# Kernel tuning notes

Hardware: AMD Instinct MI355X
Metric: run time of the kernel (lower is better)

## Reference

```python
import jax, jax.numpy as jnp
import numpy as np

SCALE = 768.0  # scale = output_features


def setup_inputs() -> dict:
    key = jax.random.key(0)
    k1, k2, k3, k4 = jax.random.split(key, 4)
    B, S, D, F = 8, 2048, 768, 768
    x = jax.random.normal(k1, (B, S, D), dtype=jnp.float32)
    # torch nn.Linear weights: shape (out_features, in_features), y = x @ W.T
    Wq = jax.random.normal(k2, (F, D), dtype=jnp.float32) * (1.0 / np.sqrt(D))
    Wk = jax.random.normal(k3, (F, D), dtype=jnp.float32) * (1.0 / np.sqrt(D))
    Wv = jax.random.normal(k4, (F, D), dtype=jnp.float32) * (1.0 / np.sqrt(D))
    return {"x": x, "Wq": Wq, "Wk": Wk, "Wv": Wv}


def _cdist_l2(q, k):
    # pairwise Euclidean distances, [B, S, S]; matches torch.cdist(q, k, p=2)
    q2 = jnp.sum(q * q, axis=-1)  # [B, S]
    k2 = jnp.sum(k * k, axis=-1)  # [B, S]
    qk = jnp.einsum('bid,bjd->bij', q, k)  # [B, S, S]
    d2 = q2[:, :, None] + k2[:, None, :] - 2.0 * qk
    return jnp.sqrt(jnp.maximum(d2, 0.0))


def reference(x, Wq, Wk, Wv):
    q = jnp.einsum('bsd,fd->bsf', x, Wq)
    k = jnp.einsum('bsd,fd->bsf', x, Wk)
    v = jnp.einsum('bsd,fd->bsf', x, Wv)
    scores = _cdist_l2(q, k) / jnp.sqrt(jnp.asarray(SCALE, dtype=x.dtype))
    attn = jax.nn.softmax(scores, axis=-1)  # NOTE: source softmaxes raw distances (no negation)
    return jnp.einsum('bij,bjf->bif', attn, v)
```

## Files before the change

### kernel.cpp

```cpp
#include <hip/hip_runtime.h>
#include <hip/hip_fp8.h>
#include <stdint.h>
#include <math.h>


typedef __attribute__((ext_vector_type(8))) __bf16 bf16x8;
typedef __attribute__((ext_vector_type(4))) float f32x4;
typedef __attribute__((ext_vector_type(4))) unsigned int u32x4;
typedef __attribute__((ext_vector_type(2))) unsigned int u32x2;

__device__ __forceinline__ unsigned short f2b(float f) {
    unsigned u = __float_as_uint(f);
    unsigned r = 0x7fffu + ((u >> 16) & 1u);
    return (unsigned short)((u + r) >> 16);
}
__device__ __forceinline__ float b2f(unsigned short h) {
    return __uint_as_float(((unsigned)h) << 16);
}
__device__ __forceinline__ unsigned char f2f8(float f) {
    __hip_fp8_e4m3 t(f);
    return t.__x;
}
__device__ __forceinline__ float f8tof(unsigned char b) {
    int e = (b >> 3) & 15, m = b & 7;
    float v = e ? ldexpf(8.0f + m, e - 10) : ldexpf((float)m, -9);
    return (b & 0x80) ? -v : v;
}

__device__ __forceinline__ void wg_barrier() {
    asm volatile("" ::: "memory");
    __builtin_amdgcn_s_barrier();
    asm volatile("" ::: "memory");
}

__device__ __forceinline__ unsigned lds_off(const void* p) {
    return (unsigned)(uintptr_t)(const __attribute__((address_space(3))) char*)p;
}

__global__ __launch_bounds__(256) void castk(const float* __restrict__ src,
                                             unsigned short* __restrict__ dst, int n4) {
    int i = blockIdx.x * 256 + threadIdx.x;
    if (i >= n4) return;
    float4 v = ((const float4*)src)[i];
    ushort4 o;
    o.x = f2b(v.x); o.y = f2b(v.y); o.z = f2b(v.z); o.w = f2b(v.w);
    ((ushort4*)dst)[i] = o;
}

template <int MODE>
__global__ __launch_bounds__(256) void rowreduce(const unsigned short* __restrict__ X,
                                                 int L, int rows, float* __restrict__ out) {
    int w = threadIdx.x >> 6, lane = threadIdx.x & 63;
    int row = blockIdx.x * 4 + w;
    if (row >= rows) return;
    const unsigned short* xr = X + (size_t)row * L;
    float s = 0.f;
    int passes = L >> 8;
    for (int p = 0; p < passes; ++p) {
        ushort4 u = *(const ushort4*)(xr + (p << 8) + lane * 4);
        float a = b2f(u.x), b = b2f(u.y), c = b2f(u.z), d = b2f(u.w);
        s += MODE ? (a * a + b * b + c * c + d * d) : (a + b + c + d);
    }
#pragma unroll
    for (int o = 32; o > 0; o >>= 1) s += __shfl_down(s, o);
    if (lane == 0) out[row] = s;
}

__global__ __launch_bounds__(256) void rowreduce8(const unsigned char* __restrict__ X,
                                                  int L, int rows, float* __restrict__ out) {
    int w = threadIdx.x >> 6, lane = threadIdx.x & 63;
    int row = blockIdx.x * 4 + w;
    if (row >= rows) return;
    const unsigned char* xr = X + (size_t)row * L;
    float s = 0.f;
    int passes = L >> 8;
    for (int p = 0; p < passes; ++p) {
        uchar4 u = *(const uchar4*)(xr + (p << 8) + lane * 4);
        float a = f8tof(u.x), b = f8tof(u.y), c = f8tof(u.z), d = f8tof(u.w);
        s += a * a + b * b + c * c + d * d;
    }
#pragma unroll
    for (int o = 32; o > 0; o >>= 1) s += __shfl_down(s, o);
    if (lane == 0) out[row] = s;
}

#define MF(A_, B_, C_) (C_) = __builtin_amdgcn_mfma_f32_16x16x32_bf16((A_), (B_), (C_), 0, 0, 0)
#define MF8(A_, B_, C_) (C_) = __builtin_amdgcn_mfma_f32_16x16x32_fp8_fp8((A_), (B_), (C_), 0, 0, 0)
#define DSR(dst_, a_, imm_) \
    asm volatile("ds_read_b128 %0, %1 offset:" #imm_ : "=v"(dst_) : "v"(a_))
#define DSR64(dst_, a_, imm_) \
    asm volatile("ds_read_b64 %0, %1 offset:" #imm_ : "=v"(dst_) : "v"(a_))
#define GL4(d_, p_) asm volatile("global_load_dwordx4 %0, %1, off" : "=v"(d_) : "v"(p_))
#define GL2(d_, p_) asm volatile("global_load_dwordx2 %0, %1, off" : "=v"(d_) : "v"(p_))
#define DSW(a_, imm_, d_) \
    asm volatile("ds_write_b128 %0, %1 offset:" #imm_ :: "v"(a_), "v"(d_) : "memory")
#define DSW64(a_, imm_, d_) \
    asm volatile("ds_write_b64 %0, %1 offset:" #imm_ :: "v"(a_), "v"(d_) : "memory")
#define LGKM(n_) asm volatile("s_waitcnt lgkmcnt(" #n_ ")" ::: "memory")
#define VMC0 asm volatile("s_waitcnt vmcnt(0)" ::: "memory")
#define SB0 __builtin_amdgcn_sched_barrier(0)

#define LOADT(T_) do {                                                     \
    const size_t ko_ = (size_t)(T_) * 64;                                  \
    GL4(ra0, pa + ko_);             GL4(ra1, pa + lda64 + ko_);            \
    GL4(ra2, pa + 2 * lda64 + ko_); GL4(ra3, pa + 3 * lda64 + ko_);        \
    GL4(rb0, pb + ko_);             GL4(rb1, pb + ldb64 + ko_);            \
    GL4(rb2, pb + 2 * ldb64 + ko_); GL4(rb3, pb + 3 * ldb64 + ko_);        \
} while (0)
#define WRITET(WB_) do {                                                   \
    const unsigned wa_ = wA + (WB_), wb2_ = wB + (WB_);                    \
    DSW(wa_, 0, ra0);     DSW(wa_, 8192, ra1);                             \
    DSW(wa_, 16384, ra2); DSW(wa_, 24576, ra3);                            \
    DSW(wb2_, 0, rb0);     DSW(wb2_, 8192, rb1);                           \
    DSW(wb2_, 16384, rb2); DSW(wb2_, 24576, rb3);                          \
} while (0)

template <int EPI>
__global__ __launch_bounds__(512, 2) void gemm256(
    const unsigned short* __restrict__ A, int lda, long long sA,
    const unsigned short* __restrict__ B, int ldb, long long sB,
    void* __restrict__ Cv, int ldc, long long sC,
    int Kd, int perm,
    const float* __restrict__ aux1, int sAux1) {
    __shared__ __attribute__((aligned(128))) unsigned short As[2 * 256 * 64];
    __shared__ __attribute__((aligned(128))) unsigned short Bs[2 * 256 * 64];

    const int z = perm ? blockIdx.x : blockIdx.z;
    const int jb = perm ? blockIdx.y : blockIdx.x;
    const int ib = perm ? blockIdx.z : blockIdx.y;
    const unsigned short* __restrict__ Ab = A + (size_t)z * sA;
    const unsigned short* __restrict__ Bb = B + (size_t)z * sB;
    const int i0 = ib * 256, j0 = jb * 256;
    const int tid = threadIdx.x;
    const int w = tid >> 6, lane = tid & 63;
    const int wr = w >> 2, wc = w & 3;
    const int c16 = lane & 15, kq = lane >> 4;

    const int lr0 = tid >> 3;
    const int clog0 = (tid & 7) ^ (lr0 & 7);
    const unsigned short* pa = Ab + (size_t)(i0 + lr0) * lda + clog0 * 8;
    const unsigned short* pb = Bb + (size_t)(j0 + lr0) * ldb + clog0 * 8;
    const size_t lda64 = (size_t)64 * lda, ldb64 = (size_t)64 * ldb;

    const unsigned wA = lds_off(As) + (unsigned)tid * 16;
    const unsigned wB = lds_off(Bs) + (unsigned)tid * 16;

    const int swc = (kq ^ (c16 & 7)) << 4;
    const unsigned adrA0 = lds_off(As) + (unsigned)(wr * 128 + c16) * 128 + swc;
    const unsigned adrA0x = adrA0 ^ 64u;
    const unsigned adrB0 = lds_off(Bs) + (unsigned)(wc * 64 + c16) * 128 + swc;
    const unsigned adrB0x = adrB0 ^ 64u;

    f32x4 acc[8][4];
    const f32x4 zero = {0.f, 0.f, 0.f, 0.f};
#pragma unroll
    for (int i = 0; i < 8; ++i)
#pragma unroll
        for (int j = 0; j < 4; ++j) acc[i][j] = zero;

    u32x4 ra0, ra1, ra2, ra3, rb0, rb1, rb2, rb3;
    bf16x8 aL[4][2], aH[4][2], bF[4][2];

    const int nt = Kd >> 6;

    LOADT(0);
    VMC0;
    WRITET(0u);
    LOADT(1);
    LGKM(0);
    wg_barrier();

    for (int t = 0; t < nt; ++t) {
        const unsigned rb_ = (t & 1) ? 32768u : 0u;
        const unsigned wb_ = (t & 1) ? 0u : 32768u;
        const unsigned aA = adrA0 + rb_, aAx = adrA0x + rb_;
        const unsigned aB = adrB0 + rb_, aBx = adrB0x + rb_;
        DSR(aL[0][0], aA, 0);    DSR(aL[0][1], aAx, 0);
        DSR(aL[1][0], aA, 2048); DSR(aL[1][1], aAx, 2048);
        DSR(aL[2][0], aA, 4096); DSR(aL[2][1], aAx, 4096);
        DSR(aL[3][0], aA, 6144); DSR(aL[3][1], aAx, 6144);
        DSR(bF[0][0], aB, 0);    DSR(bF[0][1], aBx, 0);
        DSR(bF[1][0], aB, 2048); DSR(bF[1][1], aBx, 2048);
        DSR(bF[2][0], aB, 4096); DSR(bF[2][1], aBx, 4096);
        DSR(bF[3][0], aB, 6144); DSR(bF[3][1], aBx, 6144);
        if (t + 1 < nt) {
            VMC0;
            WRITET(wb_);
            if (t + 2 < nt) LOADT(t + 2);
            LGKM(8);
        } else {
            LGKM(0);
        }
        SB0;
        __builtin_amdgcn_s_setprio(1);
#pragma unroll
        for (int kk = 0; kk < 2; ++kk)
#pragma unroll
            for (int mi = 0; mi < 4; ++mi)
#pragma unroll
                for (int ni = 0; ni < 4; ++ni)
                    MF(aL[mi][kk], bF[ni][kk], acc[mi][ni]);
        __builtin_amdgcn_s_setprio(0);
        DSR(aH[0][0], aA, 8192);  DSR(aH[0][1], aAx, 8192);
        DSR(aH[1][0], aA, 10240); DSR(aH[1][1], aAx, 10240);
        DSR(aH[2][0], aA, 12288); DSR(aH[2][1], aAx, 12288);
        DSR(aH[3][0], aA, 14336); DSR(aH[3][1], aAx, 14336);
        LGKM(0); SB0;
        __builtin_amdgcn_s_setprio(1);
#pragma unroll
        for (int kk = 0; kk < 2; ++kk)
#pragma unroll
            for (int mi = 0; mi < 4; ++mi)
#pragma unroll
                for (int ni = 0; ni < 4; ++ni)
                    MF(aH[mi][kk], bF[ni][kk], acc[4 + mi][ni]);
        __builtin_amdgcn_s_setprio(0);
        wg_barrier();
    }
    const int prow = kq * 4;
    if constexpr (EPI == 0) {
        unsigned short* C = (unsigned short*)Cv + (size_t)z * sC;
        unsigned short* sc = (unsigned short*)((char*)As + w * 8192);
        const int rr = lane >> 3, ch = lane & 7;
#pragma unroll
        for (int mi = 0; mi < 8; ++mi) {
#pragma unroll
            for (int ni = 0; ni < 4; ++ni)
#pragma unroll
                for (int r = 0; r < 4; ++r)
                    sc[(prow + r) * 72 + ni * 16 + c16] = f2b(acc[mi][ni][r]);
#pragma unroll
            for (int pass = 0; pass < 2; ++pass) {
                const int r2 = rr + 8 * pass;
                bf16x8 v = *(const bf16x8*)&sc[r2 * 72 + ch * 8];
                const int grow = i0 + wr * 128 + mi * 16 + r2;
                *(bf16x8*)&C[(size_t)grow * ldc + j0 + wc * 64 + ch * 8] = v;
            }
        }
    } else if constexpr (EPI == 3) {
        unsigned char* C = (unsigned char*)Cv + (size_t)z * sC;
        unsigned char* sc = (unsigned char*)As + w * 8192;
        const int rr = lane >> 2, ch = lane & 3;
#pragma unroll
        for (int mi = 0; mi < 8; ++mi) {
#pragma unroll
            for (int ni = 0; ni < 4; ++ni)
#pragma unroll
                for (int r = 0; r < 4; ++r)
                    sc[(prow + r) * 80 + ni * 16 + c16] = f2f8(acc[mi][ni][r]);
            u32x4 v = *(const u32x4*)&sc[rr * 80 + ch * 16];
            const int grow = i0 + wr * 128 + mi * 16 + rr;
            *(u32x4*)&C[(size_t)grow * ldc + j0 + wc * 64 + ch * 16] = v;
        }
    } else {
        float* C = (float*)Cv + (size_t)z * sC;
        const float* lb = aux1 + (size_t)z * sAux1;
        float* sc = (float*)((char*)As + w * 8192);
        const int rr = lane >> 4, ch = lane & 15;
#pragma unroll
        for (int mi = 0; mi < 8; ++mi) {
#pragma unroll
            for (int ni = 0; ni < 4; ++ni)
#pragma unroll
                for (int r = 0; r < 4; ++r) {
                    const int grow = i0 + wr * 128 + mi * 16 + prow + r;
                    sc[(prow + r) * 68 + ni * 16 + c16] = acc[mi][ni][r] / lb[grow];
                }
#pragma unroll
            for (int pass = 0; pass < 4; ++pass) {
                const int r2 = rr + 4 * pass;
                f32x4 v = *(const f32x4*)&sc[r2 * 68 + ch * 4];
                const int grow = i0 + wr * 128 + mi * 16 + r2;
                *(f32x4*)&C[(size_t)grow * ldc + j0 + wc * 64 + ch * 4] = v;
            }
        }
    }
}

#define LOADT8(T_) do {                                                    \
    const size_t ko_ = (size_t)(T_) * 64;                                  \
    GL2(fa0, pa8 + ko_);              GL2(fa1, pa8 + lda64b + ko_);        \
    GL2(fa2, pa8 + 2 * lda64b + ko_); GL2(fa3, pa8 + 3 * lda64b + ko_);    \
    GL2(fb0, pb8 + ko_);              GL2(fb1, pb8 + ldb64b + ko_);        \
    GL2(fb2, pb8 + 2 * ldb64b + ko_); GL2(fb3, pb8 + 3 * ldb64b + ko_);    \
} while (0)
#define WRITET8(WB_) do {                                                  \
    const unsigned wa_ = wA8 + (WB_), wb2_ = wB8 + (WB_);                  \
    DSW64(wa_, 0, fa0);     DSW64(wa_, 4096, fa1);                         \
    DSW64(wa_, 8192, fa2);  DSW64(wa_, 12288, fa3);                        \
    DSW64(wb2_, 0, fb0);    DSW64(wb2_, 4096, fb1);                        \
    DSW64(wb2_, 8192, fb2); DSW64(wb2_, 12288, fb3);                       \
} while (0)

__global__ __launch_bounds__(512, 2) void gemm256f8(
    const unsigned char* __restrict__ A, int lda, long long sA,
    const unsigned char* __restrict__ B, int ldb, long long sB,
    unsigned short* __restrict__ Cq, int ldc, long long sC,
    int Kd,
    const float* __restrict__ q2a, int sQ2,
    const float* __restrict__ k2a, int sK2,
    float invs) {
    __shared__ __attribute__((aligned(128))) unsigned char As8[2 * 256 * 64];
    __shared__ __attribute__((aligned(128))) unsigned char Bs8[2 * 256 * 64];

    const int z = blockIdx.x;
    const int jb = blockIdx.y, ib = blockIdx.z;
    const unsigned char* __restrict__ Ab = A + (size_t)z * sA;
    const unsigned char* __restrict__ Bb = B + (size_t)z * sB;
    const int i0 = ib * 256, j0 = jb * 256;
    const int tid = threadIdx.x;
    const int w = tid >> 6, lane = tid & 63;
    const int wr = w >> 2, wc = w & 3;
    const int c16 = lane & 15, kq = lane >> 4;

    const int lr0 = tid >> 3;
    const int slog = (tid & 7) ^ (lr0 & 7);
    const unsigned char* pa8 = Ab + (size_t)(i0 + lr0) * lda + slog * 8;
    const unsigned char* pb8 = Bb + (size_t)(j0 + lr0) * ldb + slog * 8;
    const size_t lda64b = (size_t)64 * lda, ldb64b = (size_t)64 * ldb;

    const unsigned wA8 = lds_off(As8) + (unsigned)tid * 8;
    const unsigned wB8 = lds_off(Bs8) + (unsigned)tid * 8;

    const int sw8 = (kq ^ (c16 & 7)) << 3;
    const unsigned adrA0 = lds_off(As8) + (unsigned)(wr * 128 + c16) * 64 + sw8;
    const unsigned adrA0x = adrA0 ^ 32u;
    const unsigned adrB0 = lds_off(Bs8) + (unsigned)(wc * 64 + c16) * 64 + sw8;
    const unsigned adrB0x = adrB0 ^ 32u;

    f32x4 acc[8][4];
    const f32x4 zero = {0.f, 0.f, 0.f, 0.f};
#pragma unroll
    for (int i = 0; i < 8; ++i)
#pragma unroll
        for (int j = 0; j < 4; ++j) acc[i][j] = zero;

    u32x2 fa0, fa1, fa2, fa3, fb0, fb1, fb2, fb3;
    long aL[4][2], aH[4][2], bF[4][2];

    const int nt = Kd >> 6;

    LOADT8(0);
    VMC0;
    WRITET8(0u);
    LOADT8(1);
    LGKM(0);
    wg_barrier();

    for (int t = 0; t < nt; ++t) {
        const unsigned rb_ = (t & 1) ? 16384u : 0u;
        const unsigned wb_ = (t & 1) ? 0u : 16384u;
        const unsigned aA = adrA0 + rb_, aAx = adrA0x + rb_;
        const unsigned aB = adrB0 + rb_, aBx = adrB0x + rb_;
        DSR64(aL[0][0], aA, 0);    DSR64(aL[0][1], aAx, 0);
        DSR64(aL[1][0], aA, 1024); DSR64(aL[1][1], aAx, 1024);
        DSR64(aL[2][0], aA, 2048); DSR64(aL[2][1], aAx, 2048);
        DSR64(aL[3][0], aA, 3072); DSR64(aL[3][1], aAx, 3072);
        DSR64(bF[0][0], aB, 0);    DSR64(bF[0][1], aBx, 0);
        DSR64(bF[1][0], aB, 1024); DSR64(bF[1][1], aBx, 1024);
        DSR64(bF[2][0], aB, 2048); DSR64(bF[2][1], aBx, 2048);
        DSR64(bF[3][0], aB, 3072); DSR64(bF[3][1], aBx, 3072);
        if (t + 1 < nt) {
            VMC0;
            WRITET8(wb_);
            if (t + 2 < nt) LOADT8(t + 2);
            LGKM(8);
        } else {
            LGKM(0);
        }
        SB0;
        __builtin_amdgcn_s_setprio(1);
#pragma unroll
        for (int kk = 0; kk < 2; ++kk)
#pragma unroll
            for (int mi = 0; mi < 4; ++mi)
#pragma unroll
                for (int ni = 0; ni < 4; ++ni)
                    MF8(aL[mi][kk], bF[ni][kk], acc[mi][ni]);
        __builtin_amdgcn_s_setprio(0);
        DSR64(aH[0][0], aA, 4096); DSR64(aH[0][1], aAx, 4096);
        DSR64(aH[1][0], aA, 5120); DSR64(aH[1][1], aAx, 5120);
        DSR64(aH[2][0], aA, 6144); DSR64(aH[2][1], aAx, 6144);
        DSR64(aH[3][0], aA, 7168); DSR64(aH[3][1], aAx, 7168);
        LGKM(0); SB0;
        __builtin_amdgcn_s_setprio(1);
#pragma unroll
        for (int kk = 0; kk < 2; ++kk)
#pragma unroll
            for (int mi = 0; mi < 4; ++mi)
#pragma unroll
                for (int ni = 0; ni < 4; ++ni)
                    MF8(aH[mi][kk], bF[ni][kk], acc[4 + mi][ni]);
        __builtin_amdgcn_s_setprio(0);
        wg_barrier();
    }

    unsigned short* C = Cq + (size_t)z * sC;
    const float* q2b = q2a + (size_t)z * sQ2;
    const float* k2b = k2a + (size_t)z * sK2;
    unsigned short* sc = (unsigned short*)(As8 + w * 4096);
    const int prow = kq * 4;
    const int rr = lane >> 3, ch = lane & 7;
#pragma unroll
    for (int mi = 0; mi < 8; ++mi) {
#pragma unroll
        for (int ni = 0; ni < 4; ++ni) {
            const int col = j0 + wc * 64 + ni * 16 + c16;
            const float k2v = k2b[col];
#pragma unroll
            for (int r = 0; r < 4; ++r) {
                const int grow = i0 + wr * 128 + mi * 16 + prow + r;
                float d2 = q2b[grow] + k2v - 2.0f * acc[mi][ni][r];
                float e = __expf(sqrtf(fmaxf(d2, 0.f)) * invs);
                sc[(prow + r) * 72 + ni * 16 + c16] = f2b(e);
            }
        }
#pragma unroll
        for (int pass = 0; pass < 2; ++pass) {
            const int r2 = rr + 8 * pass;
            bf16x8 v = *(const bf16x8*)&sc[r2 * 72 + ch * 8];
            const int grow = i0 + wr * 128 + mi * 16 + r2;
            *(bf16x8*)&C[(size_t)grow * ldc + j0 + wc * 64 + ch * 8] = v;
        }
    }
}

extern "C" void kernel_launch(void* const* d_in, const int* in_sizes, int n_in,
                              void* d_out, int out_size, void* d_ws, size_t ws_size,
                              hipStream_t stream) {
    const float* x = (const float*)d_in[0];
    const float* Wq = (const float*)d_in[1];
    const float* Wk = (const float*)d_in[2];
    const float* Wv = (const float*)d_in[3];
    const int Bz = 8, S = 2048, D = 768, F = 768;
    const int BS = Bz * S;

    const size_t szX = (size_t)BS * D * 2;
    const size_t szW = (size_t)F * D * 2;
    const size_t szQ8 = (size_t)BS * F;
    const size_t szE = (size_t)Bz * S * S * 2;

    char* p = (char*)d_ws;
    unsigned short* xb = (unsigned short*)p;  p += szX;
    unsigned short* Wqb = (unsigned short*)p; p += szW;
    unsigned short* Wkb = (unsigned short*)p; p += szW;
    unsigned short* Wvb = (unsigned short*)p; p += szW;
    unsigned char* Q8 = (unsigned char*)p;    p += szQ8;
    unsigned char* K8 = (unsigned char*)p;    p += szQ8;
    unsigned short* VT = (unsigned short*)p;  p += szX;
    unsigned short* E = (unsigned short*)p;   p += szE;
    float* q2 = (float*)p;   p += (size_t)BS * 4;
    float* k2 = (float*)p;   p += (size_t)BS * 4;
    float* lsum = (float*)p; p += (size_t)BS * 4;
    if ((size_t)(p - (char*)d_ws) > ws_size) return;

    const float invs = 1.0f / sqrtf(768.0f);

    castk<<<(BS * D / 4 + 255) / 256, 256, 0, stream>>>(x, xb, BS * D / 4);
    castk<<<(F * D / 4 + 255) / 256, 256, 0, stream>>>(Wq, Wqb, F * D / 4);
    castk<<<(F * D / 4 + 255) / 256, 256, 0, stream>>>(Wk, Wkb, F * D / 4);
    castk<<<(F * D / 4 + 255) / 256, 256, 0, stream>>>(Wv, Wvb, F * D / 4);

    gemm256<3><<<dim3(F / 256, BS / 256, 2), 512, 0, stream>>>(
        xb, D, 0,
        Wqb, D, (long long)F * D,
        Q8, F, (long long)BS * F,
        D, 0, nullptr, 0);

    gemm256<0><<<dim3(BS / 256, F / 256, 1), 512, 0, stream>>>(
        Wvb, D, 0,
        xb, D, 0,
        VT, BS, 0,
        D, 0, nullptr, 0);

    rowreduce8<<<BS / 4, 256, 0, stream>>>(Q8, F, BS, q2);
    rowreduce8<<<BS / 4, 256, 0, stream>>>(K8, F, BS, k2);

    gemm256f8<<<dim3(Bz, S / 256, S / 256), 512, 0, stream>>>(
        Q8, F, (long long)S * F,
        K8, F, (long long)S * F,
        E, S, (long long)S * S,
        F, q2, S, k2, S, invs);

    rowreduce<0><<<BS / 4, 256, 0, stream>>>(E, S, BS, lsum);

    gemm256<2><<<dim3(Bz, F / 256, S / 256), 512, 0, stream>>>(
        E, S, (long long)S * S,
        VT, BS, (long long)S,
        d_out, F, (long long)S * F,
        S, 1, lsum, S);
}
```

Measured before the change: 244.9 us.

## Fuse softmax row-sum into fp8 score GEMM and deepen its load pipeline

```diff
diff --git a/kernel.cpp b/kernel.cpp
--- a/kernel.cpp
+++ b/kernel.cpp
@@ -7,7 +7,6 @@
 typedef __attribute__((ext_vector_type(8))) __bf16 bf16x8;
 typedef __attribute__((ext_vector_type(4))) float f32x4;
 typedef __attribute__((ext_vector_type(4))) unsigned int u32x4;
-typedef __attribute__((ext_vector_type(2))) unsigned int u32x2;
 
 __device__ __forceinline__ unsigned short f2b(float f) {
     unsigned u = __float_as_uint(f);
@@ -47,23 +46,9 @@
     ((ushort4*)dst)[i] = o;
 }
 
-template <int MODE>
-__global__ __launch_bounds__(256) void rowreduce(const unsigned short* __restrict__ X,
-                                                 int L, int rows, float* __restrict__ out) {
-    int w = threadIdx.x >> 6, lane = threadIdx.x & 63;
-    int row = blockIdx.x * 4 + w;
-    if (row >= rows) return;
-    const unsigned short* xr = X + (size_t)row * L;
-    float s = 0.f;
-    int passes = L >> 8;
-    for (int p = 0; p < passes; ++p) {
-        ushort4 u = *(const ushort4*)(xr + (p << 8) + lane * 4);
-        float a = b2f(u.x), b = b2f(u.y), c = b2f(u.z), d = b2f(u.w);
-        s += MODE ? (a * a + b * b + c * c + d * d) : (a + b + c + d);
-    }
-#pragma unroll
-    for (int o = 32; o > 0; o >>= 1) s += __shfl_down(s, o);
-    if (lane == 0) out[row] = s;
+__global__ __launch_bounds__(256) void zerok(float* __restrict__ p, int n) {
+    int i = blockIdx.x * 256 + threadIdx.x;
+    if (i < n) p[i] = 0.f;
 }
 
 __global__ __launch_bounds__(256) void rowreduce8(const unsigned char* __restrict__ X,
@@ -91,12 +76,10 @@
 #define DSR64(dst_, a_, imm_) \
     asm volatile("ds_read_b64 %0, %1 offset:" #imm_ : "=v"(dst_) : "v"(a_))
 #define GL4(d_, p_) asm volatile("global_load_dwordx4 %0, %1, off" : "=v"(d_) : "v"(p_))
-#define GL2(d_, p_) asm volatile("global_load_dwordx2 %0, %1, off" : "=v"(d_) : "v"(p_))
 #define DSW(a_, imm_, d_) \
     asm volatile("ds_write_b128 %0, %1 offset:" #imm_ :: "v"(a_), "v"(d_) : "memory")
-#define DSW64(a_, imm_, d_) \
-    asm volatile("ds_write_b64 %0, %1 offset:" #imm_ :: "v"(a_), "v"(d_) : "memory")
 #define LGKM(n_) asm volatile("s_waitcnt lgkmcnt(" #n_ ")" ::: "memory")
+#define VMC4 asm volatile("s_waitcnt vmcnt(4)" ::: "memory")
 #define VMC0 asm volatile("s_waitcnt vmcnt(0)" ::: "memory")
 #define SB0 __builtin_amdgcn_sched_barrier(0)
 
@@ -277,19 +260,58 @@
     }
 }
 
-#define LOADT8(T_) do {                                                    \
+#define LOADT8F(T_) do {                                                   \
     const size_t ko_ = (size_t)(T_) * 64;                                  \
-    GL2(fa0, pa8 + ko_);              GL2(fa1, pa8 + lda64b + ko_);        \
-    GL2(fa2, pa8 + 2 * lda64b + ko_); GL2(fa3, pa8 + 3 * lda64b + ko_);    \
-    GL2(fb0, pb8 + ko_);              GL2(fb1, pb8 + ldb64b + ko_);        \
-    GL2(fb2, pb8 + 2 * ldb64b + ko_); GL2(fb3, pb8 + 3 * ldb64b + ko_);    \
-} while (0)
-#define WRITET8(WB_) do {                                                  \
-    const unsigned wa_ = wA8 + (WB_), wb2_ = wB8 + (WB_);                  \
-    DSW64(wa_, 0, fa0);     DSW64(wa_, 4096, fa1);                         \
-    DSW64(wa_, 8192, fa2);  DSW64(wa_, 12288, fa3);                        \
-    DSW64(wb2_, 0, fb0);    DSW64(wb2_, 4096, fb1);                        \
-    DSW64(wb2_, 8192, fb2); DSW64(wb2_, 12288, fb3);                       \
+    GL4(fa0, pa8 + ko_); GL4(fa1, pa8 + lda128 + ko_);                     \
+    GL4(fb0, pb8 + ko_); GL4(fb1, pb8 + ldb128 + ko_);                     \
+} while (0)
+#define LOADT8G(T_) do {                                                   \
+    const size_t ko_ = (size_t)(T_) * 64;                                  \
+    GL4(ga0, pa8 + ko_); GL4(ga1, pa8 + lda128 + ko_);                     \
+    GL4(gb0, pb8 + ko_); GL4(gb1, pb8 + ldb128 + ko_);                     \
+} while (0)
+#define WRITET8F(WB_) do {                                                 \
+    DSW(wA8 + (WB_), 0, fa0); DSW(wA8 + (WB_), 8192, fa1);                 \
+    DSW(wB8 + (WB_), 0, fb0); DSW(wB8 + (WB_), 8192, fb1);                 \
+} while (0)
+#define WRITET8G(WB_) do {                                                 \
+    DSW(wA8 + (WB_), 0, ga0); DSW(wA8 + (WB_), 8192, ga1);                 \
+    DSW(wB8 + (WB_), 0, gb0); DSW(wB8 + (WB_), 8192, gb1);                 \
+} while (0)
+
+#define TILE8(RB_, WB_, WSET_, LSET_, TT_) do {                            \
+    const unsigned aA = adrA80 + (RB_), aAx = aA ^ 32u;                    \
+    const unsigned aB = adrB80 + (RB_), aBx = aB ^ 32u;                    \
+    DSR64(aL[0][0], aA, 0);    DSR64(aL[0][1], aAx, 0);                    \
+    DSR64(aL[1][0], aA, 1024); DSR64(aL[1][1], aAx, 1024);                 \
+    DSR64(aL[2][0], aA, 2048); DSR64(aL[2][1], aAx, 2048);                 \
+    DSR64(aL[3][0], aA, 3072); DSR64(aL[3][1], aAx, 3072);                 \
+    DSR64(bF[0][0], aB, 0);    DSR64(bF[0][1], aBx, 0);                    \
+    DSR64(bF[1][0], aB, 1024); DSR64(bF[1][1], aBx, 1024);                 \
+    DSR64(bF[2][0], aB, 2048); DSR64(bF[2][1], aBx, 2048);                 \
+    DSR64(bF[3][0], aB, 3072); DSR64(bF[3][1], aBx, 3072);                 \
+    if ((TT_) + 3 < nt) { VMC4; WSET_(WB_); LSET_((TT_) + 3); LGKM(4); }   \
+    else if ((TT_) + 1 < nt) { VMC0; WSET_(WB_); LGKM(4); }                \
+    else { LGKM(0); }                                                      \
+    SB0;                                                                   \
+    __builtin_amdgcn_s_setprio(1);                                         \
+    _Pragma("unroll") for (int kk = 0; kk < 2; ++kk)                       \
+        _Pragma("unroll") for (int mi = 0; mi < 4; ++mi)                   \
+            _Pragma("unroll") for (int ni = 0; ni < 4; ++ni)               \
+                MF8(aL[mi][kk], bF[ni][kk], acc[mi][ni]);                  \
+    __builtin_amdgcn_s_setprio(0);                                         \
+    DSR64(aH[0][0], aA, 4096); DSR64(aH[0][1], aAx, 4096);                 \
+    DSR64(aH[1][0], aA, 5120); DSR64(aH[1][1], aAx, 5120);                 \
+    DSR64(aH[2][0], aA, 6144); DSR64(aH[2][1], aAx, 6144);                 \
+    DSR64(aH[3][0], aA, 7168); DSR64(aH[3][1], aAx, 7168);                 \
+    LGKM(0); SB0;                                                          \
+    __builtin_amdgcn_s_setprio(1);                                         \
+    _Pragma("unroll") for (int kk = 0; kk < 2; ++kk)                       \
+        _Pragma("unroll") for (int mi = 0; mi < 4; ++mi)                   \
+            _Pragma("unroll") for (int ni = 0; ni < 4; ++ni)               \
+                MF8(aH[mi][kk], bF[ni][kk], acc[4 + mi][ni]);              \
+    __builtin_amdgcn_s_setprio(0);                                         \
+    wg_barrier();                                                          \
 } while (0)
 
 __global__ __launch_bounds__(512, 2) void gemm256f8(
@@ -299,7 +321,7 @@
     int Kd,
     const float* __restrict__ q2a, int sQ2,
     const float* __restrict__ k2a, int sK2,
-    float invs) {
+    float* __restrict__ lsum, float invs) {
     __shared__ __attribute__((aligned(128))) unsigned char As8[2 * 256 * 64];
     __shared__ __attribute__((aligned(128))) unsigned char Bs8[2 * 256 * 64];
 
@@ -313,20 +335,19 @@
     const int wr = w >> 2, wc = w & 3;
     const int c16 = lane & 15, kq = lane >> 4;
 
-    const int lr0 = tid >> 3;
-    const int slog = (tid & 7) ^ (lr0 & 7);
-    const unsigned char* pa8 = Ab + (size_t)(i0 + lr0) * lda + slog * 8;
-    const unsigned char* pb8 = Bb + (size_t)(j0 + lr0) * ldb + slog * 8;
-    const size_t lda64b = (size_t)64 * lda, ldb64b = (size_t)64 * ldb;
-
-    const unsigned wA8 = lds_off(As8) + (unsigned)tid * 8;
-    const unsigned wB8 = lds_off(Bs8) + (unsigned)tid * 8;
-
-    const int sw8 = (kq ^ (c16 & 7)) << 3;
-    const unsigned adrA0 = lds_off(As8) + (unsigned)(wr * 128 + c16) * 64 + sw8;
-    const unsigned adrA0x = adrA0 ^ 32u;
-    const unsigned adrB0 = lds_off(Bs8) + (unsigned)(wc * 64 + c16) * 64 + sw8;
-    const unsigned adrB0x = adrB0 ^ 32u;
+    const int srow = tid >> 2;
+    const int p8 = (tid & 3) ^ (srow & 3) ^ ((srow >> 2) & 1);
+    const unsigned char* pa8 = Ab + (size_t)(i0 + srow) * lda + p8 * 16;
+    const unsigned char* pb8 = Bb + (size_t)(j0 + srow) * ldb + p8 * 16;
+    const size_t lda128 = (size_t)128 * lda, ldb128 = (size_t)128 * ldb;
+
+    const unsigned wA8 = lds_off(As8) + (unsigned)tid * 16;
+    const unsigned wB8 = lds_off(Bs8) + (unsigned)tid * 16;
+
+    const int gl = (c16 & 3) ^ ((c16 >> 2) & 1);
+    const int soff = ((((kq >> 1) ^ gl) << 4) | ((kq & 1) << 3));
+    const unsigned adrA80 = lds_off(As8) + (unsigned)(wr * 128 + c16) * 64 + soff;
+    const unsigned adrB80 = lds_off(Bs8) + (unsigned)(wc * 64 + c16) * 64 + soff;
 
     f32x4 acc[8][4];
     const f32x4 zero = {0.f, 0.f, 0.f, 0.f};
@@ -335,74 +356,35 @@
 #pragma unroll
         for (int j = 0; j < 4; ++j) acc[i][j] = zero;
 
-    u32x2 fa0, fa1, fa2, fa3, fb0, fb1, fb2, fb3;
+    u32x4 fa0, fa1, fb0, fb1, ga0, ga1, gb0, gb1;
     long aL[4][2], aH[4][2], bF[4][2];
 
     const int nt = Kd >> 6;
 
-    LOADT8(0);
-    VMC0;
-    WRITET8(0u);
-    LOADT8(1);
+    LOADT8F(0);
+    LOADT8G(1);
+    VMC4;
+    WRITET8F(0u);
+    LOADT8F(2);
     LGKM(0);
     wg_barrier();
 
-    for (int t = 0; t < nt; ++t) {
-        const unsigned rb_ = (t & 1) ? 16384u : 0u;
-        const unsigned wb_ = (t & 1) ? 0u : 16384u;
-        const unsigned aA = adrA0 + rb_, aAx = adrA0x + rb_;
-        const unsigned aB = adrB0 + rb_, aBx = adrB0x + rb_;
-        DSR64(aL[0][0], aA, 0);    DSR64(aL[0][1], aAx, 0);
-        DSR64(aL[1][0], aA, 1024); DSR64(aL[1][1], aAx, 1024);
-        DSR64(aL[2][0], aA, 2048); DSR64(aL[2][1], aAx, 2048);
-        DSR64(aL[3][0], aA, 3072); DSR64(aL[3][1], aAx, 3072);
-        DSR64(bF[0][0], aB, 0);    DSR64(bF[0][1], aBx, 0);
-        DSR64(bF[1][0], aB, 1024); DSR64(bF[1][1], aBx, 1024);
-        DSR64(bF[2][0], aB, 2048); DSR64(bF[2][1], aBx, 2048);
-        DSR64(bF[3][0], aB, 3072); DSR64(bF[3][1], aBx, 3072);
-        if (t + 1 < nt) {
-            VMC0;
-            WRITET8(wb_);
-            if (t + 2 < nt) LOADT8(t + 2);
-            LGKM(8);
-        } else {
-            LGKM(0);
-        }
-        SB0;
-        __builtin_amdgcn_s_setprio(1);
-#pragma unroll
-        for (int kk = 0; kk < 2; ++kk)
-#pragma unroll
-            for (int mi = 0; mi < 4; ++mi)
-#pragma unroll
-                for (int ni = 0; ni < 4; ++ni)
-                    MF8(aL[mi][kk], bF[ni][kk], acc[mi][ni]);
-        __builtin_amdgcn_s_setprio(0);
-        DSR64(aH[0][0], aA, 4096); DSR64(aH[0][1], aAx, 4096);
-        DSR64(aH[1][0], aA, 5120); DSR64(aH[1][1], aAx, 5120);
-        DSR64(aH[2][0], aA, 6144); DSR64(aH[2][1], aAx, 6144);
-        DSR64(aH[3][0], aA, 7168); DSR64(aH[3][1], aAx, 7168);
-        LGKM(0); SB0;
-        __builtin_amdgcn_s_setprio(1);
-#pragma unroll
-        for (int kk = 0; kk < 2; ++kk)
-#pragma unroll
-            for (int mi = 0; mi < 4; ++mi)
-#pragma unroll
-                for (int ni = 0; ni < 4; ++ni)
-                    MF8(aH[mi][kk], bF[ni][kk], acc[4 + mi][ni]);
-        __builtin_amdgcn_s_setprio(0);
-        wg_barrier();
+    for (int u = 0; u < nt / 2; ++u) {
+        const int t0 = 2 * u;
+        TILE8(0u, 16384u, WRITET8G, LOADT8G, t0);
+        TILE8(16384u, 0u, WRITET8F, LOADT8F, t0 + 1);
     }
 
     unsigned short* C = Cq + (size_t)z * sC;
     const float* q2b = q2a + (size_t)z * sQ2;
     const float* k2b = k2a + (size_t)z * sK2;
+    float* lz = lsum + (size_t)z * 2048;
     unsigned short* sc = (unsigned short*)(As8 + w * 4096);
     const int prow = kq * 4;
     const int rr = lane >> 3, ch = lane & 7;
 #pragma unroll
     for (int mi = 0; mi < 8; ++mi) {
+        float ev[4][4];
 #pragma unroll
         for (int ni = 0; ni < 4; ++ni) {
             const int col = j0 + wc * 64 + ni * 16 + c16;
@@ -411,10 +393,22 @@
             for (int r = 0; r < 4; ++r) {
                 const int grow = i0 + wr * 128 + mi * 16 + prow + r;
                 float d2 = q2b[grow] + k2v - 2.0f * acc[mi][ni][r];
-                float e = __expf(sqrtf(fmaxf(d2, 0.f)) * invs);
-                sc[(prow + r) * 72 + ni * 16 + c16] = f2b(e);
+                ev[ni][r] = __expf(sqrtf(fmaxf(d2, 0.f)) * invs);
             }
         }
+#pragma unroll
+        for (int r = 0; r < 4; ++r) {
+            float s = ev[0][r] + ev[1][r] + ev[2][r] + ev[3][r];
+#pragma unroll
+            for (int m = 1; m < 16; m <<= 1) s += __shfl_xor(s, m);
+            if (c16 == 0)
+                atomicAdd(lz + i0 + wr * 128 + mi * 16 + prow + r, s);
+        }
+#pragma unroll
+        for (int ni = 0; ni < 4; ++ni)
+#pragma unroll
+            for (int r = 0; r < 4; ++r)
+                sc[(prow + r) * 72 + ni * 16 + c16] = f2b(ev[ni][r]);
 #pragma unroll
         for (int pass = 0; pass < 2; ++pass) {
             const int r2 = rr + 8 * pass;
@@ -460,6 +454,7 @@
     castk<<<(F * D / 4 + 255) / 256, 256, 0, stream>>>(Wq, Wqb, F * D / 4);
     castk<<<(F * D / 4 + 255) / 256, 256, 0, stream>>>(Wk, Wkb, F * D / 4);
     castk<<<(F * D / 4 + 255) / 256, 256, 0, stream>>>(Wv, Wvb, F * D / 4);
+    zerok<<<BS / 256, 256, 0, stream>>>(lsum, BS);
 
     gemm256<3><<<dim3(F / 256, BS / 256, 2), 512, 0, stream>>>(
         xb, D, 0,
@@ -480,9 +475,7 @@
         Q8, F, (long long)S * F,
         K8, F, (long long)S * F,
         E, S, (long long)S * S,
-        F, q2, S, k2, S, invs);
-
-    rowreduce<0><<<BS / 4, 256, 0, stream>>>(E, S, BS, lsum);
+        F, q2, S, k2, S, lsum, invs);
 
     gemm256<2><<<dim3(Bz, F / 256, S / 256), 512, 0, stream>>>(
         E, S, (long long)S * S,
```

Measured after the change: 240.6 us. About the same (-1.7%).

## Fuse softmax row-sum into distance GEMM epilogue, drop separate rowreduce pass

Applied to the files above, without the earlier changes.

```diff
diff --git a/kernel.cpp b/kernel.cpp
--- a/kernel.cpp
+++ b/kernel.cpp
@@ -45,25 +45,6 @@
     ushort4 o;
     o.x = f2b(v.x); o.y = f2b(v.y); o.z = f2b(v.z); o.w = f2b(v.w);
     ((ushort4*)dst)[i] = o;
-}
-
-template <int MODE>
-__global__ __launch_bounds__(256) void rowreduce(const unsigned short* __restrict__ X,
-                                                 int L, int rows, float* __restrict__ out) {
-    int w = threadIdx.x >> 6, lane = threadIdx.x & 63;
-    int row = blockIdx.x * 4 + w;
-    if (row >= rows) return;
-    const unsigned short* xr = X + (size_t)row * L;
-    float s = 0.f;
-    int passes = L >> 8;
-    for (int p = 0; p < passes; ++p) {
-        ushort4 u = *(const ushort4*)(xr + (p << 8) + lane * 4);
-        float a = b2f(u.x), b = b2f(u.y), c = b2f(u.z), d = b2f(u.w);
-        s += MODE ? (a * a + b * b + c * c + d * d) : (a + b + c + d);
-    }
-#pragma unroll
-    for (int o = 32; o > 0; o >>= 1) s += __shfl_down(s, o);
-    if (lane == 0) out[row] = s;
 }
 
 __global__ __launch_bounds__(256) void rowreduce8(const unsigned char* __restrict__ X,
@@ -254,18 +235,25 @@
         }
     } else {
         float* C = (float*)Cv + (size_t)z * sC;
-        const float* lb = aux1 + (size_t)z * sAux1;
+        const float* lp = aux1 + (size_t)z * 8 * 2048;
         float* sc = (float*)((char*)As + w * 8192);
         const int rr = lane >> 4, ch = lane & 15;
 #pragma unroll
         for (int mi = 0; mi < 8; ++mi) {
+            float linv[4];
+#pragma unroll
+            for (int r = 0; r < 4; ++r) {
+                const int grow = i0 + wr * 128 + mi * 16 + prow + r;
+                float s = 0.f;
+#pragma unroll
+                for (int j = 0; j < 8; ++j) s += lp[j * 2048 + grow];
+                linv[r] = 1.0f / s;
+            }
 #pragma unroll
             for (int ni = 0; ni < 4; ++ni)
 #pragma unroll
-                for (int r = 0; r < 4; ++r) {
-                    const int grow = i0 + wr * 128 + mi * 16 + prow + r;
-                    sc[(prow + r) * 68 + ni * 16 + c16] = acc[mi][ni][r] / lb[grow];
-                }
+                for (int r = 0; r < 4; ++r)
+                    sc[(prow + r) * 68 + ni * 16 + c16] = acc[mi][ni][r] * linv[r];
 #pragma unroll
             for (int pass = 0; pass < 4; ++pass) {
                 const int r2 = rr + 4 * pass;
@@ -299,7 +287,7 @@
     int Kd,
     const float* __restrict__ q2a, int sQ2,
     const float* __restrict__ k2a, int sK2,
-    float invs) {
+    float* __restrict__ lpart, float invs) {
     __shared__ __attribute__((aligned(128))) unsigned char As8[2 * 256 * 64];
     __shared__ __attribute__((aligned(128))) unsigned char Bs8[2 * 256 * 64];
 
@@ -399,10 +387,12 @@
     const float* q2b = q2a + (size_t)z * sQ2;
     const float* k2b = k2a + (size_t)z * sK2;
     unsigned short* sc = (unsigned short*)(As8 + w * 4096);
+    float* lred = (float*)Bs8;
     const int prow = kq * 4;
     const int rr = lane >> 3, ch = lane & 7;
 #pragma unroll
     for (int mi = 0; mi < 8; ++mi) {
+        float ev[4][4];
 #pragma unroll
         for (int ni = 0; ni < 4; ++ni) {
             const int col = j0 + wc * 64 + ni * 16 + c16;
@@ -411,16 +401,40 @@
             for (int r = 0; r < 4; ++r) {
                 const int grow = i0 + wr * 128 + mi * 16 + prow + r;
                 float d2 = q2b[grow] + k2v - 2.0f * acc[mi][ni][r];
-                float e = __expf(sqrtf(fmaxf(d2, 0.f)) * invs);
-                sc[(prow + r) * 72 + ni * 16 + c16] = f2b(e);
+                ev[ni][r] = __expf(sqrtf(fmaxf(d2, 0.f)) * invs);
             }
         }
+#pragma unroll
+        for (int r = 0; r < 4; ++r) {
+            float s = ev[0][r] + ev[1][r] + ev[2][r] + ev[3][r];
+#pragma unroll
+            for (int m = 1; m < 16; m <<= 1) s += __shfl_xor(s, m);
+            if (c16 == 0)
+                lred[(wr * 4 + wc) * 128 + mi * 16 + prow + r] = s;
+        }
+#pragma unroll
+        for (int ni = 0; ni < 4; ++ni)
+#pragma unroll
+            for (int r = 0; r < 4; ++r)
+                sc[(prow + r) * 72 + ni * 16 + c16] = f2b(ev[ni][r]);
 #pragma unroll
         for (int pass = 0; pass < 2; ++pass) {
             const int r2 = rr + 8 * pass;
             bf16x8 v = *(const bf16x8*)&sc[r2 * 72 + ch * 8];
             const int grow = i0 + wr * 128 + mi * 16 + r2;
             *(bf16x8*)&C[(size_t)grow * ldc + j0 + wc * 64 + ch * 8] = v;
+        }
+    }
+    LGKM(0);
+    wg_barrier();
+    if (wc == 0) {
+        float* lrow = lpart + ((size_t)z * 8 + jb) * 2048 + i0 + wr * 128;
+#pragma unroll
+        for (int h = 0; h < 2; ++h) {
+            const int row = lane + h * 64;
+            float s = lred[(wr * 4 + 0) * 128 + row] + lred[(wr * 4 + 1) * 128 + row] +
+                      lred[(wr * 4 + 2) * 128 + row] + lred[(wr * 4 + 3) * 128 + row];
+            lrow[row] = s;
         }
     }
 }
@@ -449,9 +463,9 @@
     unsigned char* K8 = (unsigned char*)p;    p += szQ8;
     unsigned short* VT = (unsigned short*)p;  p += szX;
     unsigned short* E = (unsigned short*)p;   p += szE;
-    float* q2 = (float*)p;   p += (size_t)BS * 4;
-    float* k2 = (float*)p;   p += (size_t)BS * 4;
-    float* lsum = (float*)p; p += (size_t)BS * 4;
+    float* q2 = (float*)p;    p += (size_t)BS * 4;
+    float* k2 = (float*)p;    p += (size_t)BS * 4;
+    float* lpart = (float*)p; p += (size_t)Bz * 8 * 2048 * 4;
     if ((size_t)(p - (char*)d_ws) > ws_size) return;
 
     const float invs = 1.0f / sqrtf(768.0f);
@@ -480,13 +494,11 @@
         Q8, F, (long long)S * F,
         K8, F, (long long)S * F,
         E, S, (long long)S * S,
-        F, q2, S, k2, S, invs);
-
-    rowreduce<0><<<BS / 4, 256, 0, stream>>>(E, S, BS, lsum);
+        F, q2, S, k2, S, lpart, invs);
 
     gemm256<2><<<dim3(Bz, F / 256, S / 256), 512, 0, stream>>>(
         E, S, (long long)S * S,
         VT, BS, (long long)S,
         d_out, F, (long long)S * F,
-        S, 1, lsum, S);
-}
+        S, 1, lpart, 0);
+}
```

Result: no change. 241.7 us (-1.3%).

## Shrink FP8 distance GEMM tile to 128x256 with 16-byte loads and occupancy 4

Applied to the files above, without the earlier changes.

```diff
diff --git a/kernel.cpp b/kernel.cpp
--- a/kernel.cpp
+++ b/kernel.cpp
@@ -7,7 +7,6 @@
 typedef __attribute__((ext_vector_type(8))) __bf16 bf16x8;
 typedef __attribute__((ext_vector_type(4))) float f32x4;
 typedef __attribute__((ext_vector_type(4))) unsigned int u32x4;
-typedef __attribute__((ext_vector_type(2))) unsigned int u32x2;
 
 __device__ __forceinline__ unsigned short f2b(float f) {
     unsigned u = __float_as_uint(f);
@@ -91,11 +90,8 @@
 #define DSR64(dst_, a_, imm_) \
     asm volatile("ds_read_b64 %0, %1 offset:" #imm_ : "=v"(dst_) : "v"(a_))
 #define GL4(d_, p_) asm volatile("global_load_dwordx4 %0, %1, off" : "=v"(d_) : "v"(p_))
-#define GL2(d_, p_) asm volatile("global_load_dwordx2 %0, %1, off" : "=v"(d_) : "v"(p_))
 #define DSW(a_, imm_, d_) \
     asm volatile("ds_write_b128 %0, %1 offset:" #imm_ :: "v"(a_), "v"(d_) : "memory")
-#define DSW64(a_, imm_, d_) \
-    asm volatile("ds_write_b64 %0, %1 offset:" #imm_ :: "v"(a_), "v"(d_) : "memory")
 #define LGKM(n_) asm volatile("s_waitcnt lgkmcnt(" #n_ ")" ::: "memory")
 #define VMC0 asm volatile("s_waitcnt vmcnt(0)" ::: "memory")
 #define SB0 __builtin_amdgcn_sched_barrier(0)
@@ -279,20 +275,15 @@
 
 #define LOADT8(T_) do {                                                    \
     const size_t ko_ = (size_t)(T_) * 64;                                  \
-    GL2(fa0, pa8 + ko_);              GL2(fa1, pa8 + lda64b + ko_);        \
-    GL2(fa2, pa8 + 2 * lda64b + ko_); GL2(fa3, pa8 + 3 * lda64b + ko_);    \
-    GL2(fb0, pb8 + ko_);              GL2(fb1, pb8 + ldb64b + ko_);        \
-    GL2(fb2, pb8 + 2 * ldb64b + ko_); GL2(fb3, pb8 + 3 * ldb64b + ko_);    \
+    GL4(fa0, pa8 + ko_);                                                   \
+    GL4(fb0, pb8 + ko_); GL4(fb1, pb8 + ldb128 + ko_);                     \
 } while (0)
 #define WRITET8(WB_) do {                                                  \
-    const unsigned wa_ = wA8 + (WB_), wb2_ = wB8 + (WB_);                  \
-    DSW64(wa_, 0, fa0);     DSW64(wa_, 4096, fa1);                         \
-    DSW64(wa_, 8192, fa2);  DSW64(wa_, 12288, fa3);                        \
-    DSW64(wb2_, 0, fb0);    DSW64(wb2_, 4096, fb1);                        \
-    DSW64(wb2_, 8192, fb2); DSW64(wb2_, 12288, fb3);                       \
+    DSW(wA8 + ((WB_) >> 1), 0, fa0);                                       \
+    DSW(wB8 + (WB_), 0, fb0); DSW(wB8 + (WB_), 8192, fb1);                 \
 } while (0)
 
-__global__ __launch_bounds__(512, 2) void gemm256f8(
+__global__ __launch_bounds__(512, 4) void gemm256f8(
     const unsigned char* __restrict__ A, int lda, long long sA,
     const unsigned char* __restrict__ B, int ldb, long long sB,
     unsigned short* __restrict__ Cq, int ldc, long long sC,
@@ -300,43 +291,42 @@
     const float* __restrict__ q2a, int sQ2,
     const float* __restrict__ k2a, int sK2,
     float invs) {
-    __shared__ __attribute__((aligned(128))) unsigned char As8[2 * 256 * 64];
+    __shared__ __attribute__((aligned(128))) unsigned char As8[2 * 128 * 64];
     __shared__ __attribute__((aligned(128))) unsigned char Bs8[2 * 256 * 64];
 
     const int z = blockIdx.x;
     const int jb = blockIdx.y, ib = blockIdx.z;
     const unsigned char* __restrict__ Ab = A + (size_t)z * sA;
     const unsigned char* __restrict__ Bb = B + (size_t)z * sB;
-    const int i0 = ib * 256, j0 = jb * 256;
+    const int i0 = ib * 128, j0 = jb * 256;
     const int tid = threadIdx.x;
     const int w = tid >> 6, lane = tid & 63;
     const int wr = w >> 2, wc = w & 3;
     const int c16 = lane & 15, kq = lane >> 4;
 
-    const int lr0 = tid >> 3;
-    const int slog = (tid & 7) ^ (lr0 & 7);
-    const unsigned char* pa8 = Ab + (size_t)(i0 + lr0) * lda + slog * 8;
-    const unsigned char* pb8 = Bb + (size_t)(j0 + lr0) * ldb + slog * 8;
-    const size_t lda64b = (size_t)64 * lda, ldb64b = (size_t)64 * ldb;
-
-    const unsigned wA8 = lds_off(As8) + (unsigned)tid * 8;
-    const unsigned wB8 = lds_off(Bs8) + (unsigned)tid * 8;
-
-    const int sw8 = (kq ^ (c16 & 7)) << 3;
-    const unsigned adrA0 = lds_off(As8) + (unsigned)(wr * 128 + c16) * 64 + sw8;
-    const unsigned adrA0x = adrA0 ^ 32u;
-    const unsigned adrB0 = lds_off(Bs8) + (unsigned)(wc * 64 + c16) * 64 + sw8;
-    const unsigned adrB0x = adrB0 ^ 32u;
-
-    f32x4 acc[8][4];
+    const int srow = tid >> 2;
+    const int p8 = (tid & 3) ^ (srow & 3) ^ ((srow >> 2) & 1);
+    const unsigned char* pa8 = Ab + (size_t)(i0 + srow) * lda + p8 * 16;
+    const unsigned char* pb8 = Bb + (size_t)(j0 + srow) * ldb + p8 * 16;
+    const size_t ldb128 = (size_t)128 * ldb;
+
+    const unsigned wA8 = lds_off(As8) + (unsigned)tid * 16;
+    const unsigned wB8 = lds_off(Bs8) + (unsigned)tid * 16;
+
+    const int gl = (c16 & 3) ^ ((c16 >> 2) & 1);
+    const int soff = ((((kq >> 1) ^ gl) << 4) | ((kq & 1) << 3));
+    const unsigned adrA80 = lds_off(As8) + (unsigned)(wr * 64 + c16) * 64 + soff;
+    const unsigned adrB80 = lds_off(Bs8) + (unsigned)(wc * 64 + c16) * 64 + soff;
+
+    f32x4 acc[4][4];
     const f32x4 zero = {0.f, 0.f, 0.f, 0.f};
 #pragma unroll
-    for (int i = 0; i < 8; ++i)
+    for (int i = 0; i < 4; ++i)
 #pragma unroll
         for (int j = 0; j < 4; ++j) acc[i][j] = zero;
 
-    u32x2 fa0, fa1, fa2, fa3, fb0, fb1, fb2, fb3;
-    long aL[4][2], aH[4][2], bF[4][2];
+    u32x4 fa0, fb0, fb1;
+    long aF[4][2], bF[4][2];
 
     const int nt = Kd >> 6;
 
@@ -350,12 +340,12 @@
     for (int t = 0; t < nt; ++t) {
         const unsigned rb_ = (t & 1) ? 16384u : 0u;
         const unsigned wb_ = (t & 1) ? 0u : 16384u;
-        const unsigned aA = adrA0 + rb_, aAx = adrA0x + rb_;
-        const unsigned aB = adrB0 + rb_, aBx = adrB0x + rb_;
-        DSR64(aL[0][0], aA, 0);    DSR64(aL[0][1], aAx, 0);
-        DSR64(aL[1][0], aA, 1024); DSR64(aL[1][1], aAx, 1024);
-        DSR64(aL[2][0], aA, 2048); DSR64(aL[2][1], aAx, 2048);
-        DSR64(aL[3][0], aA, 3072); DSR64(aL[3][1], aAx, 3072);
+        const unsigned aA = adrA80 + (rb_ >> 1), aAx = aA ^ 32u;
+        const unsigned aB = adrB80 + rb_, aBx = aB ^ 32u;
+        DSR64(aF[0][0], aA, 0);    DSR64(aF[0][1], aAx, 0);
+        DSR64(aF[1][0], aA, 1024); DSR64(aF[1][1], aAx, 1024);
+        DSR64(aF[2][0], aA, 2048); DSR64(aF[2][1], aAx, 2048);
+        DSR64(aF[3][0], aA, 3072); DSR64(aF[3][1], aAx, 3072);
         DSR64(bF[0][0], aB, 0);    DSR64(bF[0][1], aBx, 0);
         DSR64(bF[1][0], aB, 1024); DSR64(bF[1][1], aBx, 1024);
         DSR64(bF[2][0], aB, 2048); DSR64(bF[2][1], aBx, 2048);
@@ -364,7 +354,7 @@
             VMC0;
             WRITET8(wb_);
             if (t + 2 < nt) LOADT8(t + 2);
-            LGKM(8);
+            LGKM(3);
         } else {
             LGKM(0);
         }
@@ -376,40 +366,27 @@
             for (int mi = 0; mi < 4; ++mi)
 #pragma unroll
                 for (int ni = 0; ni < 4; ++ni)
-                    MF8(aL[mi][kk], bF[ni][kk], acc[mi][ni]);
+                    MF8(aF[mi][kk], bF[ni][kk], acc[mi][ni]);
         __builtin_amdgcn_s_setprio(0);
-        DSR64(aH[0][0], aA, 4096); DSR64(aH[0][1], aAx, 4096);
-        DSR64(aH[1][0], aA, 5120); DSR64(aH[1][1], aAx, 5120);
-        DSR64(aH[2][0], aA, 6144); DSR64(aH[2][1], aAx, 6144);
-        DSR64(aH[3][0], aA, 7168); DSR64(aH[3][1], aAx, 7168);
-        LGKM(0); SB0;
-        __builtin_amdgcn_s_setprio(1);
-#pragma unroll
-        for (int kk = 0; kk < 2; ++kk)
-#pragma unroll
-            for (int mi = 0; mi < 4; ++mi)
-#pragma unroll
-                for (int ni = 0; ni < 4; ++ni)
-                    MF8(aH[mi][kk], bF[ni][kk], acc[4 + mi][ni]);
-        __builtin_amdgcn_s_setprio(0);
+        LGKM(0);
         wg_barrier();
     }
 
     unsigned short* C = Cq + (size_t)z * sC;
     const float* q2b = q2a + (size_t)z * sQ2;
     const float* k2b = k2a + (size_t)z * sK2;
-    unsigned short* sc = (unsigned short*)(As8 + w * 4096);
+    unsigned short* sc = (unsigned short*)(Bs8 + w * 4096);
     const int prow = kq * 4;
     const int rr = lane >> 3, ch = lane & 7;
 #pragma unroll
-    for (int mi = 0; mi < 8; ++mi) {
+    for (int mi = 0; mi < 4; ++mi) {
 #pragma unroll
         for (int ni = 0; ni < 4; ++ni) {
             const int col = j0 + wc * 64 + ni * 16 + c16;
             const float k2v = k2b[col];
 #pragma unroll
             for (int r = 0; r < 4; ++r) {
-                const int grow = i0 + wr * 128 + mi * 16 + prow + r;
+                const int grow = i0 + wr * 64 + mi * 16 + prow + r;
                 float d2 = q2b[grow] + k2v - 2.0f * acc[mi][ni][r];
                 float e = __expf(sqrtf(fmaxf(d2, 0.f)) * invs);
                 sc[(prow + r) * 72 + ni * 16 + c16] = f2b(e);
@@ -419,7 +396,7 @@
         for (int pass = 0; pass < 2; ++pass) {
             const int r2 = rr + 8 * pass;
             bf16x8 v = *(const bf16x8*)&sc[r2 * 72 + ch * 8];
-            const int grow = i0 + wr * 128 + mi * 16 + r2;
+            const int grow = i0 + wr * 64 + mi * 16 + r2;
             *(bf16x8*)&C[(size_t)grow * ldc + j0 + wc * 64 + ch * 8] = v;
         }
     }
@@ -449,9 +426,9 @@
     unsigned char* K8 = (unsigned char*)p;    p += szQ8;
     unsigned short* VT = (unsigned short*)p;  p += szX;
     unsigned short* E = (unsigned short*)p;   p += szE;
-    float* q2 = (float*)p;   p += (size_t)BS * 4;
-    float* k2 = (float*)p;   p += (size_t)BS * 4;
-    float* lsum = (float*)p; p += (size_t)BS * 4;
+    float* q2 = (float*)p;    p += (size_t)BS * 4;
+    float* k2 = (float*)p;    p += (size_t)BS * 4;
+    float* lsum = (float*)p;  p += (size_t)BS * 4;
     if ((size_t)(p - (char*)d_ws) > ws_size) return;
 
     const float invs = 1.0f / sqrtf(768.0f);
@@ -476,7 +453,7 @@
     rowreduce8<<<BS / 4, 256, 0, stream>>>(Q8, F, BS, q2);
     rowreduce8<<<BS / 4, 256, 0, stream>>>(K8, F, BS, k2);
 
-    gemm256f8<<<dim3(Bz, S / 256, S / 256), 512, 0, stream>>>(
+    gemm256f8<<<dim3(Bz, S / 256, S / 128), 512, 0, stream>>>(
         Q8, F, (long long)S * F,
         K8, F, (long long)S * F,
         E, S, (long long)S * S,
```

Result: faster. 233.1 us (-4.8%).
